# Performance work log

Measured on AMD Instinct MI355X. Metric: run time of the kernel, lower is better.

The kernel has to match this reference:

```python
import jax, jax.numpy as jnp
import numpy as np

B, E, C = 512, 512, 100000
S, M, LAMDA, ALPHA = 30.0, 0.35, 0.01, 0.5  # s, m, lamda from init; ALPHA = args.alpha (center lr)
EPS = 1e-6


def setup_inputs() -> dict:
    key = jax.random.key(0)
    k1, k2, k3, k4 = jax.random.split(key, 4)
    embedding = jax.random.normal(k1, (B, E), dtype=jnp.float32)
    weights = jax.random.normal(k2, (C, E), dtype=jnp.float32)  # kaiming-init classifier weights
    centers = jax.random.normal(k3, (C, E), dtype=jnp.float32)  # class centers buffer
    label = jax.random.randint(k4, (B,), 0, C, dtype=jnp.int64)
    return {"embedding": embedding, "weights": weights, "centers": centers, "label": label}


def reference(embedding, weights, centers, label):
    rows = jnp.arange(B)
    # LMCL (CosFace) logits: cosine similarity via L2-normalized features and weights
    emb_n = embedding / jnp.linalg.norm(embedding, axis=1, keepdims=True)
    w_n = weights / jnp.linalg.norm(weights, axis=1, keepdims=True)
    logits = jnp.einsum('be,ce->bc', emb_n, w_n)            # [B, C]
    # subtract margin m at the target class, then scale by s
    m_logits = S * logits.at[rows, label].add(-M)
    logp = jax.nn.log_softmax(m_logits, axis=1)
    lmcl_loss = -jnp.mean(logp[rows, label])
    # top-1 precision (%)
    prec = jnp.mean((jnp.argmax(m_logits, axis=1) == label).astype(jnp.float32)) * 100.0
    # center loss: MSE between features and their class centers (centers treated as constant)
    centers_batch = centers[label]                           # [B, E] gather
    center_loss = jnp.mean((embedding - centers_batch) ** 2)
    # center update: scatter-subtract mean-normalized diff (replaces the python loop)
    counts = jnp.zeros((C,), dtype=jnp.float32).at[label].add(1.0)
    appear = counts[label]                                   # [B]
    diff = ALPHA * (centers_batch - embedding) / (appear[:, None] + EPS)
    new_centers = centers.at[label].add(-diff)
    total_loss = lmcl_loss + LAMDA * center_loss
    return prec, total_loss, new_centers
```

## Files before the change

### kernel.cpp

```cpp
#include <hip/hip_runtime.h>
#include <cstdint>
#include <cstddef>

#define B_ROWS 512
#define E_DIM  512
#define C_CLS  100000
#define NT     782

#define S_SC    30.0f
#define M_MRG   0.35f
#define LAMBDA_ 0.01f
#define ALPHA_  0.5f
#define EPS_    1e-6f

#define BM 128
#define BN 128
#define BK 64
#define LPAD 8

#define GBN    128
#define GBK    32
#define GSTEPS 16
#define A_GRAN 2048
#define SLOT_GRAN 2560

typedef __attribute__((ext_vector_type(8))) short bf16x8;
typedef __attribute__((ext_vector_type(4))) float f32x4;

static_assert((size_t)NT * GBN >= C_CLS, "tile count");

constexpr size_t WS_PSUM  = 0;
constexpr size_t WS_PMAX  = WS_PSUM + (size_t)NT * B_ROWS * 4;
constexpr size_t WS_CLOSS = WS_PMAX + (size_t)NT * B_ROWS * 4;
constexpr size_t WS_EMBN  = WS_CLOSS + 512;
constexpr size_t WS_IEN   = WS_EMBN + (size_t)B_ROWS * E_DIM * 2;
constexpr size_t WS_COSL  = WS_IEN + 2048;
constexpr size_t WS_CNT   = WS_COSL + 2048;
constexpr size_t WS_RSUM  = WS_CNT + 2048;
constexpr size_t WS_RMAX  = WS_RSUM + 2048;
constexpr size_t WS_WBF   = 4 * 1024 * 1024;
constexpr size_t WS_NEED  = WS_WBF + (size_t)C_CLS * E_DIM * 2;

__device__ __forceinline__ unsigned short f2bf(float f) {
    unsigned u = __float_as_uint(f);
    u += 0x7fffu + ((u >> 16) & 1u);
    return (unsigned short)(u >> 16);
}
__device__ __forceinline__ unsigned fkey(float f) {
    unsigned u = __float_as_uint(f);
    return (u & 0x80000000u) ? ~u : (u | 0x80000000u);
}
__device__ __forceinline__ float unkey(unsigned k) {
    unsigned u = (k & 0x80000000u) ? (k ^ 0x80000000u) : ~k;
    return __uint_as_float(u);
}
__device__ __forceinline__ float waveReduceSum(float v) {
#pragma unroll
    for (int d = 1; d < 64; d <<= 1) v += __shfl_xor(v, d, 64);
    return v;
}
__device__ __forceinline__ unsigned waveReduceMax(unsigned v) {
#pragma unroll
    for (int d = 1; d < 64; d <<= 1) { unsigned o = __shfl_xor(v, d, 64); v = o > v ? o : v; }
    return v;
}
__device__ __forceinline__ float blockReduceSum256(float v, float* s4) {
    v = waveReduceSum(v);
    int w = threadIdx.x >> 6;
    if ((threadIdx.x & 63) == 0) s4[w] = v;
    __syncthreads();
    float r = s4[0] + s4[1] + s4[2] + s4[3];
    __syncthreads();
    return r;
}
__device__ __forceinline__ void g2l16(const void* g, void* l) {
    __builtin_amdgcn_global_load_lds(
        (const __attribute__((address_space(1))) unsigned int*)g,
        (__attribute__((address_space(3))) unsigned int*)l, 16, 0, 0);
}


__global__ __launch_bounds__(256) void emb_prep(const float* __restrict__ emb,
                                                unsigned short* __restrict__ embn,
                                                float* __restrict__ ien) {
    __shared__ float s4[4];
    int b = blockIdx.x, t = threadIdx.x;
    float2 v = *(const float2*)(emb + (size_t)b * E_DIM + t * 2);
    float ss = blockReduceSum256(v.x * v.x + v.y * v.y, s4);
    float inv = 1.0f / sqrtf(ss);
    ushort2 o; o.x = f2bf(v.x * inv); o.y = f2bf(v.y * inv);
    *(ushort2*)(embn + (size_t)b * E_DIM + t * 2) = o;
    if (t == 0) ien[b] = inv;
}

__global__ __launch_bounds__(256) void w_prep(const float* __restrict__ W,
                                              unsigned short* __restrict__ wbf) {
    int row = blockIdx.x * 4 + (threadIdx.x >> 6);
    int lane = threadIdx.x & 63;
    const float* src = W + (size_t)row * E_DIM;
    f32x4 a = *(const f32x4*)(src + lane * 4);
    f32x4 b = *(const f32x4*)(src + 256 + lane * 4);
    float ss = a.x*a.x + a.y*a.y + a.z*a.z + a.w*a.w
             + b.x*b.x + b.y*b.y + b.z*b.z + b.w*b.w;
    ss = waveReduceSum(ss);
    float inv = 1.0f / sqrtf(fmaxf(ss, 1e-30f));
    ushort4 o0, o1;
    o0.x = f2bf(a.x*inv); o0.y = f2bf(a.y*inv); o0.z = f2bf(a.z*inv); o0.w = f2bf(a.w*inv);
    o1.x = f2bf(b.x*inv); o1.y = f2bf(b.y*inv); o1.z = f2bf(b.z*inv); o1.w = f2bf(b.w*inv);
    *(ushort4*)(wbf + (size_t)row * E_DIM + lane * 4) = o0;
    *(ushort4*)(wbf + (size_t)row * E_DIM + 256 + lane * 4) = o1;
}

__global__ __launch_bounds__(256) void label_stats(const float* __restrict__ emb,
                                                   const float* __restrict__ W,
                                                   const float* __restrict__ centers,
                                                   const int* __restrict__ label,
                                                   const float* __restrict__ ien,
                                                   float* __restrict__ cosl,
                                                   float* __restrict__ cntf,
                                                   float* __restrict__ closs) {
    __shared__ float s4[4];
    int b = blockIdx.x, t = threadIdx.x;
    int lab = label[b];
    float d = 0.f, wss = 0.f, sq = 0.f;
    for (int c = t; c < E_DIM; c += 256) {
        float e  = emb[(size_t)b * E_DIM + c];
        float w  = W[(size_t)lab * E_DIM + c];
        float ce = centers[(size_t)lab * E_DIM + c];
        d += e * w; wss += w * w;
        float df = e - ce; sq += df * df;
    }
    float cn = ((label[t] == lab) ? 1.f : 0.f) + ((label[t + 256] == lab) ? 1.f : 0.f);
    d   = blockReduceSum256(d, s4);
    wss = blockReduceSum256(wss, s4);
    sq  = blockReduceSum256(sq, s4);
    cn  = blockReduceSum256(cn, s4);
    if (t == 0) {
        cosl[b] = d * ien[b] / sqrtf(wss);
        cntf[b] = cn;
        atomicAdd(closs, sq);
    }
}

__global__ __launch_bounds__(512, 1) void gemm_fast(const unsigned short* __restrict__ embn,
                                                    const unsigned short* __restrict__ wbf,
                                                    const int* __restrict__ label,
                                                    float* __restrict__ psum,
                                                    unsigned* __restrict__ pmax) {
    __shared__ __align__(16) unsigned short sbuf[3][SLOT_GRAN * 8];
    __shared__ int sLab[B_ROWS];

    const int tid  = threadIdx.x;
    const int lane = tid & 63, wave = tid >> 6;
    const int wm = wave >> 1, wn = wave & 1;
    const int q = lane >> 4, lm = lane & 15;
    const int n0 = blockIdx.x * GBN;

    if (tid < B_ROWS) sLab[tid] = label[tid];

    const int swz = (tid & 3) ^ ((tid >> 3) & 3);
    int aOff[4];
#pragma unroll
    for (int j = 0; j < 4; ++j) {
        int r = j * 128 + (tid >> 2);
        aOff[j] = r * (E_DIM * 2) + swz * 16;
    }
    int rb = n0 + (tid >> 2); if (rb >= C_CLS) rb = 0;
    const size_t bOff = (size_t)rb * (E_DIM * 2) + (size_t)swz * 16;

    const char* aBase = (const char*)embn;
    const char* bBase = (const char*)wbf;

    f32x4 acc[8][4];
#pragma unroll
    for (int i = 0; i < 8; ++i)
#pragma unroll
        for (int j = 0; j < 4; ++j) acc[i][j] = (f32x4){0.f, 0.f, 0.f, 0.f};

#pragma unroll
    for (int s = 0; s < 2; ++s) {
        unsigned short* d = &sbuf[s][0];
        const int kb = s * (GBK * 2);
#pragma unroll
        for (int j = 0; j < 4; ++j)
            g2l16(aBase + aOff[j] + kb, d + (j * 512 + wave * 64) * 8);
        g2l16(bBase + bOff + kb, d + (A_GRAN + wave * 64) * 8);
    }

    const int pq16 = (q ^ ((lm >> 1) & 3)) * 16;

    int sc = 0, ss = 2;
    for (int t = 0; t < GSTEPS; ++t) {
        if (t < GSTEPS - 1)
            asm volatile("s_waitcnt vmcnt(5) lgkmcnt(0)\n\ts_barrier" ::: "memory");
        else
            asm volatile("s_waitcnt vmcnt(0) lgkmcnt(0)\n\ts_barrier" ::: "memory");

        const char* sb = (const char*)&sbuf[sc][0];
        bf16x8 af[8], bfr[4];
#pragma unroll
        for (int i = 0; i < 8; ++i)
            af[i] = *(const bf16x8*)(sb + (wm * 128 + i * 16 + lm) * 64 + pq16);
#pragma unroll
        for (int j = 0; j < 4; ++j)
            bfr[j] = *(const bf16x8*)(sb + A_GRAN * 16 + (wn * 64 + j * 16 + lm) * 64 + pq16);
#pragma unroll
        for (int i = 0; i < 8; ++i)
#pragma unroll
            for (int j = 0; j < 4; ++j)
                acc[i][j] = __builtin_amdgcn_mfma_f32_16x16x32_bf16(af[i], bfr[j], acc[i][j], 0, 0, 0);

        if (t + 2 < GSTEPS) {
            unsigned short* d = &sbuf[ss][0];
            const int kb = (t + 2) * (GBK * 2);
#pragma unroll
            for (int j = 0; j < 4; ++j)
                g2l16(aBase + aOff[j] + kb, d + (j * 512 + wave * 64) * 8);
            g2l16(bBase + bOff + kb, d + (A_GRAN + wave * 64) * 8);
        }
        sc = (sc == 2) ? 0 : sc + 1;
        ss = (ss == 2) ? 0 : ss + 1;
    }

    const size_t pbase = (size_t)blockIdx.x * B_ROWS;
#pragma unroll
    for (int i = 0; i < 8; ++i) {
#pragma unroll
        for (int r = 0; r < 4; ++r) {
            int row = wm * 128 + i * 16 + q * 4 + r;
            int lab = sLab[row];
            float sum = 0.f, mx = -1e30f;
#pragma unroll
            for (int j = 0; j < 4; ++j) {
                int col = n0 + wn * 64 + j * 16 + lm;
                float v = S_SC * acc[i][j][r];
                if (col < C_CLS && col != lab) {
                    sum += __expf(v - 30.0f);
                    mx = fmaxf(mx, v);
                }
            }
#pragma unroll
            for (int d = 1; d < 16; d <<= 1) {
                sum += __shfl_xor(sum, d, 64);
                mx = fmaxf(mx, __shfl_xor(mx, d, 64));
            }
            if (lm == 0) {
                atomicAdd(&psum[pbase + row], sum);
                atomicMax(&pmax[pbase + row], fkey(mx));
            }
        }
    }
}

__global__ __launch_bounds__(256) void gemm_slow(const unsigned short* __restrict__ embn,
                                                 const float* __restrict__ W,
                                                 const int* __restrict__ label,
                                                 float* __restrict__ psum,
                                                 unsigned* __restrict__ pmax) {
    __shared__ __align__(16) unsigned short sA[BM][BK + LPAD];
    __shared__ __align__(16) unsigned short sB[BN][BK + LPAD];
    __shared__ int      sLab[BM];
    __shared__ float    sSum[BM];
    __shared__ unsigned sMax[BM];
    __shared__ float    sInvN[BN];

    const int tid = threadIdx.x;
    const int m0 = blockIdx.x * BM;
    const int n0 = blockIdx.y * BN;
    if (tid < BM) { sLab[tid] = label[m0 + tid]; sSum[tid] = 0.f; sMax[tid] = 0u; }

    const int lane = tid & 63;
    const int wave = tid >> 6;
    const int wm = wave >> 1, wn = wave & 1;
    const int q = lane >> 4, lm = lane & 15;

    const int arow = tid >> 3, ac8 = tid & 7;
    const int brow = tid >> 4, bc4 = tid & 15;

    f32x4 acc[4][4];
#pragma unroll
    for (int i = 0; i < 4; ++i)
#pragma unroll
        for (int j = 0; j < 4; ++j) acc[i][j] = (f32x4){0.f, 0.f, 0.f, 0.f};

    float rss[8];
#pragma unroll
    for (int j = 0; j < 8; ++j) rss[j] = 0.f;

    const float* wb = W + (size_t)(n0 + brow) * E_DIM + bc4 * 4;

    for (int k0 = 0; k0 < E_DIM; k0 += BK) {
        __syncthreads();
#pragma unroll
        for (int j = 0; j < 4; ++j) {
            int rr = arow + 32 * j;
            uint4 v = *(const uint4*)(embn + (size_t)(m0 + rr) * E_DIM + k0 + ac8 * 8);
            *(uint4*)(&sA[rr][ac8 * 8]) = v;
        }
#pragma unroll
        for (int j = 0; j < 8; ++j) {
            int rr = brow + 16 * j;
            f32x4 v = (f32x4){0.f, 0.f, 0.f, 0.f};
            if (n0 + rr < C_CLS) v = *(const f32x4*)(wb + (size_t)(16 * j) * E_DIM + k0);
            rss[j] += v.x * v.x + v.y * v.y + v.z * v.z + v.w * v.w;
            ushort4 o; o.x = f2bf(v.x); o.y = f2bf(v.y); o.z = f2bf(v.z); o.w = f2bf(v.w);
            *(ushort4*)(&sB[rr][bc4 * 4]) = o;
        }
        __syncthreads();
#pragma unroll
        for (int kk = 0; kk < BK; kk += 32) {
            bf16x8 af[4], bfr[4];
#pragma unroll
            for (int i = 0; i < 4; ++i)
                af[i] = *(const bf16x8*)(&sA[wm * 64 + i * 16 + lm][kk + q * 8]);
#pragma unroll
            for (int j = 0; j < 4; ++j)
                bfr[j] = *(const bf16x8*)(&sB[wn * 64 + j * 16 + lm][kk + q * 8]);
#pragma unroll
            for (int i = 0; i < 4; ++i)
#pragma unroll
                for (int j = 0; j < 4; ++j)
                    acc[i][j] = __builtin_amdgcn_mfma_f32_16x16x32_bf16(af[i], bfr[j], acc[i][j], 0, 0, 0);
        }
    }
#pragma unroll
    for (int j = 0; j < 8; ++j) {
        float v = rss[j];
#pragma unroll
        for (int d = 1; d < 16; d <<= 1) v += __shfl_xor(v, d, 64);
        if (bc4 == 0) sInvN[brow + 16 * j] = rsqrtf(fmaxf(v, 1e-30f));
    }
    __syncthreads();
#pragma unroll
    for (int i = 0; i < 4; ++i) {
#pragma unroll
        for (int r = 0; r < 4; ++r) {
            int row_l = wm * 64 + i * 16 + q * 4 + r;
            int lab = sLab[row_l];
            float sum = 0.f, mx = -1e30f;
#pragma unroll
            for (int j = 0; j < 4; ++j) {
                int col_l = wn * 64 + j * 16 + lm;
                int col = n0 + col_l;
                float v = S_SC * acc[i][j][r] * sInvN[col_l];
                if (col < C_CLS && col != lab) {
                    sum += __expf(v - 30.0f);
                    mx = fmaxf(mx, v);
                }
            }
#pragma unroll
            for (int d = 1; d < 16; d <<= 1) {
                sum += __shfl_xor(sum, d, 64);
                mx = fmaxf(mx, __shfl_xor(mx, d, 64));
            }
            if (lm == 0) {
                atomicAdd(&sSum[row_l], sum);
                atomicMax(&sMax[row_l], fkey(mx));
            }
        }
    }
    __syncthreads();
    if (tid < BM) {
        psum[(size_t)blockIdx.y * B_ROWS + m0 + tid] = sSum[tid];
        pmax[(size_t)blockIdx.y * B_ROWS + m0 + tid] = sMax[tid];
    }
}

__global__ __launch_bounds__(256) void row_reduce(const float* __restrict__ psum,
                                                  const unsigned* __restrict__ pmax,
                                                  float* __restrict__ rsum,
                                                  float* __restrict__ rmax) {
    __shared__ float s4[4];
    __shared__ unsigned m4[4];
    int b = blockIdx.x, t = threadIdx.x;
    float s = 0.f; unsigned mk = 0u;
    for (int nt = t; nt < NT; nt += 256) {
        s += psum[(size_t)nt * B_ROWS + b];
        unsigned k = pmax[(size_t)nt * B_ROWS + b];
        mk = k > mk ? k : mk;
    }
    s = waveReduceSum(s);
    mk = waveReduceMax(mk);
    int w = t >> 6;
    if ((t & 63) == 0) { s4[w] = s; m4[w] = mk; }
    __syncthreads();
    if (t == 0) {
        rsum[b] = s4[0] + s4[1] + s4[2] + s4[3];
        unsigned m = m4[0];
#pragma unroll
        for (int i = 1; i < 4; ++i) m = m4[i] > m ? m4[i] : m;
        rmax[b] = unkey(m);
    }
}

__global__ __launch_bounds__(256) void finalize(const float* __restrict__ cosl,
                                                const float* __restrict__ rsum,
                                                const float* __restrict__ rmax,
                                                const float* __restrict__ closs,
                                                float* __restrict__ out) {
    __shared__ float s4[4];
    int t = threadIdx.x;
    float lsum = 0.f, msum = 0.f;
    for (int b = t; b < B_ROWS; b += 256) {
        float lv = S_SC * (cosl[b] - M_MRG);
        float tot = rsum[b] + __expf(lv - 30.0f);
        lsum += (logf(tot) + 30.0f) - lv;
        msum += (lv > rmax[b]) ? 1.0f : 0.0f;
    }
    lsum = blockReduceSum256(lsum, s4);
    msum = blockReduceSum256(msum, s4);
    if (t == 0) {
        out[0] = msum * (100.0f / (float)B_ROWS);
        out[1] = lsum * (1.0f / (float)B_ROWS)
               + LAMBDA_ * closs[0] * (1.0f / ((float)B_ROWS * (float)E_DIM));
    }
}

__global__ __launch_bounds__(256) void centers_copy(const float* __restrict__ src,
                                                    float* __restrict__ dst) {
    size_t i = (size_t)blockIdx.x * blockDim.x + threadIdx.x;
    size_t stride = (size_t)gridDim.x * blockDim.x;
    constexpr size_t N  = (size_t)C_CLS * E_DIM;
    constexpr size_t n4 = (N - 2) / 4;
    const float2* s2 = (const float2*)(src + 2);
    float4* d4 = (float4*)(dst + 2);
    for (size_t k = i; k < n4; k += stride) {
        float2 a = s2[2 * k], b = s2[2 * k + 1];
        d4[k] = make_float4(a.x, a.y, b.x, b.y);
    }
    if (i == 0) {
        *(float2*)dst = *(const float2*)src;
        constexpr size_t t0 = 2 + 4 * n4;
        *(float2*)(dst + t0) = *(const float2*)(src + t0);
    }
}

__global__ __launch_bounds__(256) void scatter_upd(const float* __restrict__ emb,
                                                   const float* __restrict__ centers,
                                                   const int* __restrict__ label,
                                                   const float* __restrict__ cntf,
                                                   float* __restrict__ outC) {
    int b = blockIdx.x, t = threadIdx.x;
    int lab = label[b];
    float sc = ALPHA_ / (cntf[b] + EPS_);
    for (int c = t; c < E_DIM; c += 256) {
        float add = sc * (emb[(size_t)b * E_DIM + c] - centers[(size_t)lab * E_DIM + c]);
        atomicAdd(outC + (size_t)lab * E_DIM + c, add);
    }
}

extern "C" void kernel_launch(void* const* d_in, const int* in_sizes, int n_in,
                              void* d_out, int out_size, void* d_ws, size_t ws_size,
                              hipStream_t stream) {
    const float* emb     = (const float*)d_in[0];
    const float* W       = (const float*)d_in[1];
    const float* centers = (const float*)d_in[2];
    const int*   label   = (const int*)d_in[3];
    float* out = (float*)d_out;
    char* ws = (char*)d_ws;

    float*          psum = (float*)(ws + WS_PSUM);
    unsigned*       pmax = (unsigned*)(ws + WS_PMAX);
    float*          closs = (float*)(ws + WS_CLOSS);
    unsigned short* embn = (unsigned short*)(ws + WS_EMBN);
    float*          ien  = (float*)(ws + WS_IEN);
    float*          cosl = (float*)(ws + WS_COSL);
    float*          cntf = (float*)(ws + WS_CNT);
    float*          rsum = (float*)(ws + WS_RSUM);
    float*          rmax = (float*)(ws + WS_RMAX);
    unsigned short* wbf  = (unsigned short*)(ws + WS_WBF);

    hipMemsetAsync(ws, 0, WS_CLOSS + 512, stream);

    emb_prep<<<B_ROWS, 256, 0, stream>>>(emb, embn, ien);
    label_stats<<<B_ROWS, 256, 0, stream>>>(emb, W, centers, label, ien, cosl, cntf, closs);
    if (ws_size >= WS_NEED) {
        w_prep<<<C_CLS / 4, 256, 0, stream>>>(W, wbf);
        gemm_fast<<<NT, 512, 0, stream>>>(embn, wbf, label, psum, pmax);
    } else {
        gemm_slow<<<dim3(B_ROWS / BM, NT), 256, 0, stream>>>(embn, W, label, psum, pmax);
    }
    row_reduce<<<B_ROWS, 256, 0, stream>>>(psum, pmax, rsum, rmax);
    finalize<<<1, 256, 0, stream>>>(cosl, rsum, rmax, closs, out);
    centers_copy<<<12500, 256, 0, stream>>>(centers, out + 2);
    scatter_upd<<<B_ROWS, 256, 0, stream>>>(emb, centers, label, cntf, out + 2);
}
```

Baseline: 602.5 us.

## Fuse weight normalization and centers copy into GEMM, drop bf16 weight prepass

```diff
diff --git a/kernel.cpp b/kernel.cpp
--- a/kernel.cpp
+++ b/kernel.cpp
@@ -13,16 +13,8 @@
 #define ALPHA_  0.5f
 #define EPS_    1e-6f
 
-#define BM 128
-#define BN 128
-#define BK 64
-#define LPAD 8
-
 #define GBN    128
-#define GBK    32
 #define GSTEPS 16
-#define A_GRAN 2048
-#define SLOT_GRAN 2560
 
 typedef __attribute__((ext_vector_type(8))) short bf16x8;
 typedef __attribute__((ext_vector_type(4))) float f32x4;
@@ -33,13 +25,10 @@
 constexpr size_t WS_PMAX  = WS_PSUM + (size_t)NT * B_ROWS * 4;
 constexpr size_t WS_CLOSS = WS_PMAX + (size_t)NT * B_ROWS * 4;
 constexpr size_t WS_EMBN  = WS_CLOSS + 512;
-constexpr size_t WS_IEN   = WS_EMBN + (size_t)B_ROWS * E_DIM * 2;
-constexpr size_t WS_COSL  = WS_IEN + 2048;
+constexpr size_t WS_COSL  = WS_EMBN + (size_t)B_ROWS * E_DIM * 2;
 constexpr size_t WS_CNT   = WS_COSL + 2048;
 constexpr size_t WS_RSUM  = WS_CNT + 2048;
 constexpr size_t WS_RMAX  = WS_RSUM + 2048;
-constexpr size_t WS_WBF   = 4 * 1024 * 1024;
-constexpr size_t WS_NEED  = WS_WBF + (size_t)C_CLS * E_DIM * 2;
 
 __device__ __forceinline__ unsigned short f2bf(float f) {
     unsigned u = __float_as_uint(f);
@@ -73,82 +62,55 @@
     __syncthreads();
     return r;
 }
-__device__ __forceinline__ void g2l16(const void* g, void* l) {
-    __builtin_amdgcn_global_load_lds(
-        (const __attribute__((address_space(1))) unsigned int*)g,
-        (__attribute__((address_space(3))) unsigned int*)l, 16, 0, 0);
-}
-
-
-__global__ __launch_bounds__(256) void emb_prep(const float* __restrict__ emb,
-                                                unsigned short* __restrict__ embn,
-                                                float* __restrict__ ien) {
-    __shared__ float s4[4];
-    int b = blockIdx.x, t = threadIdx.x;
-    float2 v = *(const float2*)(emb + (size_t)b * E_DIM + t * 2);
-    float ss = blockReduceSum256(v.x * v.x + v.y * v.y, s4);
-    float inv = 1.0f / sqrtf(ss);
-    ushort2 o; o.x = f2bf(v.x * inv); o.y = f2bf(v.y * inv);
-    *(ushort2*)(embn + (size_t)b * E_DIM + t * 2) = o;
-    if (t == 0) ien[b] = inv;
-}
-
-__global__ __launch_bounds__(256) void w_prep(const float* __restrict__ W,
-                                              unsigned short* __restrict__ wbf) {
-    int row = blockIdx.x * 4 + (threadIdx.x >> 6);
-    int lane = threadIdx.x & 63;
-    const float* src = W + (size_t)row * E_DIM;
-    f32x4 a = *(const f32x4*)(src + lane * 4);
-    f32x4 b = *(const f32x4*)(src + 256 + lane * 4);
-    float ss = a.x*a.x + a.y*a.y + a.z*a.z + a.w*a.w
-             + b.x*b.x + b.y*b.y + b.z*b.z + b.w*b.w;
-    ss = waveReduceSum(ss);
-    float inv = 1.0f / sqrtf(fmaxf(ss, 1e-30f));
-    ushort4 o0, o1;
-    o0.x = f2bf(a.x*inv); o0.y = f2bf(a.y*inv); o0.z = f2bf(a.z*inv); o0.w = f2bf(a.w*inv);
-    o1.x = f2bf(b.x*inv); o1.y = f2bf(b.y*inv); o1.z = f2bf(b.z*inv); o1.w = f2bf(b.w*inv);
-    *(ushort4*)(wbf + (size_t)row * E_DIM + lane * 4) = o0;
-    *(ushort4*)(wbf + (size_t)row * E_DIM + 256 + lane * 4) = o1;
-}
-
-__global__ __launch_bounds__(256) void label_stats(const float* __restrict__ emb,
-                                                   const float* __restrict__ W,
-                                                   const float* __restrict__ centers,
-                                                   const int* __restrict__ label,
-                                                   const float* __restrict__ ien,
-                                                   float* __restrict__ cosl,
-                                                   float* __restrict__ cntf,
-                                                   float* __restrict__ closs) {
+
+
+__global__ __launch_bounds__(256) void prep_stats(const float* __restrict__ emb,
+                                                  const float* __restrict__ W,
+                                                  const float* __restrict__ centers,
+                                                  const int* __restrict__ label,
+                                                  unsigned short* __restrict__ embn,
+                                                  float* __restrict__ cosl,
+                                                  float* __restrict__ cntf,
+                                                  float* __restrict__ closs) {
     __shared__ float s4[4];
     int b = blockIdx.x, t = threadIdx.x;
     int lab = label[b];
-    float d = 0.f, wss = 0.f, sq = 0.f;
-    for (int c = t; c < E_DIM; c += 256) {
-        float e  = emb[(size_t)b * E_DIM + c];
-        float w  = W[(size_t)lab * E_DIM + c];
-        float ce = centers[(size_t)lab * E_DIM + c];
-        d += e * w; wss += w * w;
-        float df = e - ce; sq += df * df;
-    }
+    float2 e2 = *(const float2*)(emb     + (size_t)b   * E_DIM + t * 2);
+    float2 w2 = *(const float2*)(W       + (size_t)lab * E_DIM + t * 2);
+    float2 c2 = *(const float2*)(centers + (size_t)lab * E_DIM + t * 2);
+    float ssq = e2.x * e2.x + e2.y * e2.y;
+    float d   = e2.x * w2.x + e2.y * w2.y;
+    float wss = w2.x * w2.x + w2.y * w2.y;
+    float dx = e2.x - c2.x, dy = e2.y - c2.y;
+    float sq  = dx * dx + dy * dy;
     float cn = ((label[t] == lab) ? 1.f : 0.f) + ((label[t + 256] == lab) ? 1.f : 0.f);
-    d   = blockReduceSum256(d, s4);
+    ssq = blockReduceSum256(ssq, s4);
+    d   = blockReduceSum256(d,   s4);
     wss = blockReduceSum256(wss, s4);
-    sq  = blockReduceSum256(sq, s4);
-    cn  = blockReduceSum256(cn, s4);
+    sq  = blockReduceSum256(sq,  s4);
+    cn  = blockReduceSum256(cn,  s4);
+    float inv = 1.0f / sqrtf(ssq);
+    ushort2 o; o.x = f2bf(e2.x * inv); o.y = f2bf(e2.y * inv);
+    *(ushort2*)(embn + (size_t)b * E_DIM + t * 2) = o;
     if (t == 0) {
-        cosl[b] = d * ien[b] / sqrtf(wss);
+        cosl[b] = d * inv / sqrtf(wss);
         cntf[b] = cn;
         atomicAdd(closs, sq);
     }
 }
 
-__global__ __launch_bounds__(512, 1) void gemm_fast(const unsigned short* __restrict__ embn,
-                                                    const unsigned short* __restrict__ wbf,
-                                                    const int* __restrict__ label,
-                                                    float* __restrict__ psum,
-                                                    unsigned* __restrict__ pmax) {
-    __shared__ __align__(16) unsigned short sbuf[3][SLOT_GRAN * 8];
-    __shared__ int sLab[B_ROWS];
+__global__ __launch_bounds__(512, 1) void gemm_fused(const unsigned short* __restrict__ embn,
+                                                     const float* __restrict__ W,
+                                                     const int* __restrict__ label,
+                                                     float* __restrict__ psum,
+                                                     unsigned* __restrict__ pmax,
+                                                     const float* __restrict__ centers,
+                                                     float* __restrict__ outC,
+                                                     unsigned* __restrict__ ctr) {
+    __shared__ __align__(16) unsigned short sB[2][GBN * 32];
+    __shared__ int      sLab[B_ROWS];
+    __shared__ float    sInv[GBN];
+    __shared__ unsigned sChunk;
 
     const int tid  = threadIdx.x;
     const int lane = tid & 63, wave = tid >> 6;
@@ -156,20 +118,26 @@
     const int q = lane >> 4, lm = lane & 15;
     const int n0 = blockIdx.x * GBN;
 
-    if (tid < B_ROWS) sLab[tid] = label[tid];
-
-    const int swz = (tid & 3) ^ ((tid >> 3) & 3);
-    int aOff[4];
+    sLab[tid & (B_ROWS - 1)] = label[tid & (B_ROWS - 1)];
+
+    const int brow = tid >> 2;
+    const int bl   = tid & 3;
+    int brg = n0 + brow; if (brg >= C_CLS) brg = 0;
+    const float* bsrc = W + (size_t)brg * E_DIM + bl * 8;
+    const int bphys = bl ^ ((brow >> 1) & 3);
+    unsigned short* bwr = &sB[0][brow * 32 + bphys * 8];
+
+    const unsigned short* aP[8];
+#pragma unroll
+    for (int i = 0; i < 8; ++i)
+        aP[i] = embn + (size_t)(wm * 128 + i * 16 + lm) * E_DIM + q * 8;
+
+    const unsigned short* brd[4];
 #pragma unroll
     for (int j = 0; j < 4; ++j) {
-        int r = j * 128 + (tid >> 2);
-        aOff[j] = r * (E_DIM * 2) + swz * 16;
-    }
-    int rb = n0 + (tid >> 2); if (rb >= C_CLS) rb = 0;
-    const size_t bOff = (size_t)rb * (E_DIM * 2) + (size_t)swz * 16;
-
-    const char* aBase = (const char*)embn;
-    const char* bBase = (const char*)wbf;
+        int row = wn * 64 + j * 16 + lm;
+        brd[j] = &sB[0][row * 32 + (q ^ ((row >> 1) & 3)) * 8];
+    }
 
     f32x4 acc[8][4];
 #pragma unroll
@@ -177,50 +145,78 @@
 #pragma unroll
         for (int j = 0; j < 4; ++j) acc[i][j] = (f32x4){0.f, 0.f, 0.f, 0.f};
 
-#pragma unroll
-    for (int s = 0; s < 2; ++s) {
-        unsigned short* d = &sbuf[s][0];
-        const int kb = s * (GBK * 2);
-#pragma unroll
-        for (int j = 0; j < 4; ++j)
-            g2l16(aBase + aOff[j] + kb, d + (j * 512 + wave * 64) * 8);
-        g2l16(bBase + bOff + kb, d + (A_GRAN + wave * 64) * 8);
-    }
-
-    const int pq16 = (q ^ ((lm >> 1) & 3)) * 16;
-
-    int sc = 0, ss = 2;
-    for (int t = 0; t < GSTEPS; ++t) {
-        if (t < GSTEPS - 1)
-            asm volatile("s_waitcnt vmcnt(5) lgkmcnt(0)\n\ts_barrier" ::: "memory");
-        else
-            asm volatile("s_waitcnt vmcnt(0) lgkmcnt(0)\n\ts_barrier" ::: "memory");
-
-        const char* sb = (const char*)&sbuf[sc][0];
-        bf16x8 af[8], bfr[4];
-#pragma unroll
-        for (int i = 0; i < 8; ++i)
-            af[i] = *(const bf16x8*)(sb + (wm * 128 + i * 16 + lm) * 64 + pq16);
-#pragma unroll
-        for (int j = 0; j < 4; ++j)
-            bfr[j] = *(const bf16x8*)(sb + A_GRAN * 16 + (wn * 64 + j * 16 + lm) * 64 + pq16);
-#pragma unroll
-        for (int i = 0; i < 8; ++i)
-#pragma unroll
-            for (int j = 0; j < 4; ++j)
-                acc[i][j] = __builtin_amdgcn_mfma_f32_16x16x32_bf16(af[i], bfr[j], acc[i][j], 0, 0, 0);
-
-        if (t + 2 < GSTEPS) {
-            unsigned short* d = &sbuf[ss][0];
-            const int kb = (t + 2) * (GBK * 2);
-#pragma unroll
-            for (int j = 0; j < 4; ++j)
-                g2l16(aBase + aOff[j] + kb, d + (j * 512 + wave * 64) * 8);
-            g2l16(bBase + bOff + kb, d + (A_GRAN + wave * 64) * 8);
-        }
-        sc = (sc == 2) ? 0 : sc + 1;
-        ss = (ss == 2) ? 0 : ss + 1;
-    }
+    float ss = 0.f;
+    f32x4 bA0, bA1, bB0, bB1;
+
+    bA0 = *(const f32x4*)(bsrc + 0);
+    bA1 = *(const f32x4*)(bsrc + 4);
+    bB0 = *(const f32x4*)(bsrc + 32);
+    bB1 = *(const f32x4*)(bsrc + 36);
+    {
+        ss += bA0.x*bA0.x + bA0.y*bA0.y + bA0.z*bA0.z + bA0.w*bA0.w
+            + bA1.x*bA1.x + bA1.y*bA1.y + bA1.z*bA1.z + bA1.w*bA1.w;
+        bf16x8 o;
+        o[0] = (short)f2bf(bA0.x); o[1] = (short)f2bf(bA0.y);
+        o[2] = (short)f2bf(bA0.z); o[3] = (short)f2bf(bA0.w);
+        o[4] = (short)f2bf(bA1.x); o[5] = (short)f2bf(bA1.y);
+        o[6] = (short)f2bf(bA1.z); o[7] = (short)f2bf(bA1.w);
+        *(bf16x8*)bwr = o;
+    }
+    asm volatile("s_waitcnt lgkmcnt(0)" ::: "memory");
+    __builtin_amdgcn_sched_barrier(0);
+    __builtin_amdgcn_s_barrier();
+
+#define STEP(T, WR0, WR1, LD0, LD1)                                             \
+    {                                                                           \
+        const int t_ = (T);                                                     \
+        bf16x8 af[8];                                                           \
+        _Pragma("unroll")                                                       \
+        for (int i = 0; i < 8; ++i)                                             \
+            af[i] = *(const bf16x8*)(aP[i] + t_ * 32);                          \
+        if (t_ + 2 < GSTEPS) {                                                  \
+            LD0 = *(const f32x4*)(bsrc + (t_ + 2) * 32);                        \
+            LD1 = *(const f32x4*)(bsrc + (t_ + 2) * 32 + 4);                    \
+        }                                                                       \
+        if (t_ + 1 < GSTEPS) {                                                  \
+            ss += WR0.x*WR0.x + WR0.y*WR0.y + WR0.z*WR0.z + WR0.w*WR0.w         \
+                + WR1.x*WR1.x + WR1.y*WR1.y + WR1.z*WR1.z + WR1.w*WR1.w;        \
+            bf16x8 o;                                                           \
+            o[0] = (short)f2bf(WR0.x); o[1] = (short)f2bf(WR0.y);               \
+            o[2] = (short)f2bf(WR0.z); o[3] = (short)f2bf(WR0.w);               \
+            o[4] = (short)f2bf(WR1.x); o[5] = (short)f2bf(WR1.y);               \
+            o[6] = (short)f2bf(WR1.z); o[7] = (short)f2bf(WR1.w);               \
+            *(bf16x8*)(bwr + ((t_ + 1) & 1) * 4096) = o;                        \
+        }                                                                       \
+        bf16x8 bfr[4];                                                          \
+        _Pragma("unroll")                                                       \
+        for (int j = 0; j < 4; ++j)                                             \
+            bfr[j] = *(const bf16x8*)(brd[j] + (t_ & 1) * 4096);                \
+        _Pragma("unroll")                                                       \
+        for (int i = 0; i < 8; ++i)                                             \
+            _Pragma("unroll")                                                   \
+            for (int j = 0; j < 4; ++j)                                         \
+                acc[i][j] = __builtin_amdgcn_mfma_f32_16x16x32_bf16(af[i], bfr[j], acc[i][j], 0, 0, 0); \
+        __builtin_amdgcn_sched_barrier(0);                                      \
+        asm volatile("s_waitcnt lgkmcnt(0)" ::: "memory");                      \
+        __builtin_amdgcn_sched_barrier(0);                                      \
+        __builtin_amdgcn_s_barrier();                                           \
+    }
+
+#pragma unroll
+    for (int tt = 0; tt < GSTEPS; tt += 2) {
+        STEP(tt,     bB0, bB1, bA0, bA1);
+        STEP(tt + 1, bA0, bA1, bB0, bB1);
+    }
+#undef STEP
+
+    ss += __shfl_xor(ss, 1, 64);
+    ss += __shfl_xor(ss, 2, 64);
+    if ((tid & 3) == 0) sInv[brow] = rsqrtf(fmaxf(ss, 1e-30f));
+    __syncthreads();
+
+    float inv_j[4];
+#pragma unroll
+    for (int j = 0; j < 4; ++j) inv_j[j] = sInv[wn * 64 + j * 16 + lm];
 
     const size_t pbase = (size_t)blockIdx.x * B_ROWS;
 #pragma unroll
@@ -233,7 +229,7 @@
 #pragma unroll
             for (int j = 0; j < 4; ++j) {
                 int col = n0 + wn * 64 + j * 16 + lm;
-                float v = S_SC * acc[i][j][r];
+                float v = S_SC * acc[i][j][r] * inv_j[j];
                 if (col < C_CLS && col != lab) {
                     sum += __expf(v - 30.0f);
                     mx = fmaxf(mx, v);
@@ -250,119 +246,31 @@
             }
         }
     }
-}
-
-__global__ __launch_bounds__(256) void gemm_slow(const unsigned short* __restrict__ embn,
-                                                 const float* __restrict__ W,
-                                                 const int* __restrict__ label,
-                                                 float* __restrict__ psum,
-                                                 unsigned* __restrict__ pmax) {
-    __shared__ __align__(16) unsigned short sA[BM][BK + LPAD];
-    __shared__ __align__(16) unsigned short sB[BN][BK + LPAD];
-    __shared__ int      sLab[BM];
-    __shared__ float    sSum[BM];
-    __shared__ unsigned sMax[BM];
-    __shared__ float    sInvN[BN];
-
-    const int tid = threadIdx.x;
-    const int m0 = blockIdx.x * BM;
-    const int n0 = blockIdx.y * BN;
-    if (tid < BM) { sLab[tid] = label[m0 + tid]; sSum[tid] = 0.f; sMax[tid] = 0u; }
-
-    const int lane = tid & 63;
-    const int wave = tid >> 6;
-    const int wm = wave >> 1, wn = wave & 1;
-    const int q = lane >> 4, lm = lane & 15;
-
-    const int arow = tid >> 3, ac8 = tid & 7;
-    const int brow = tid >> 4, bc4 = tid & 15;
-
-    f32x4 acc[4][4];
-#pragma unroll
-    for (int i = 0; i < 4; ++i)
-#pragma unroll
-        for (int j = 0; j < 4; ++j) acc[i][j] = (f32x4){0.f, 0.f, 0.f, 0.f};
-
-    float rss[8];
-#pragma unroll
-    for (int j = 0; j < 8; ++j) rss[j] = 0.f;
-
-    const float* wb = W + (size_t)(n0 + brow) * E_DIM + bc4 * 4;
-
-    for (int k0 = 0; k0 < E_DIM; k0 += BK) {
+
+    constexpr size_t N4 = ((size_t)C_CLS * E_DIM - 2) / 4;
+    constexpr unsigned NCHUNK = (unsigned)((N4 + 4095) / 4096);
+    const float2* s2 = (const float2*)(centers + 2);
+    float4* d4 = (float4*)(outC + 2);
+    for (;;) {
+        if (tid == 0) sChunk = atomicAdd(ctr, 1u);
         __syncthreads();
-#pragma unroll
-        for (int j = 0; j < 4; ++j) {
-            int rr = arow + 32 * j;
-            uint4 v = *(const uint4*)(embn + (size_t)(m0 + rr) * E_DIM + k0 + ac8 * 8);
-            *(uint4*)(&sA[rr][ac8 * 8]) = v;
-        }
-#pragma unroll
-        for (int j = 0; j < 8; ++j) {
-            int rr = brow + 16 * j;
-            f32x4 v = (f32x4){0.f, 0.f, 0.f, 0.f};
-            if (n0 + rr < C_CLS) v = *(const f32x4*)(wb + (size_t)(16 * j) * E_DIM + k0);
-            rss[j] += v.x * v.x + v.y * v.y + v.z * v.z + v.w * v.w;
-            ushort4 o; o.x = f2bf(v.x); o.y = f2bf(v.y); o.z = f2bf(v.z); o.w = f2bf(v.w);
-            *(ushort4*)(&sB[rr][bc4 * 4]) = o;
-        }
+        unsigned c = sChunk;
         __syncthreads();
-#pragma unroll
-        for (int kk = 0; kk < BK; kk += 32) {
-            bf16x8 af[4], bfr[4];
-#pragma unroll
-            for (int i = 0; i < 4; ++i)
-                af[i] = *(const bf16x8*)(&sA[wm * 64 + i * 16 + lm][kk + q * 8]);
-#pragma unroll
-            for (int j = 0; j < 4; ++j)
-                bfr[j] = *(const bf16x8*)(&sB[wn * 64 + j * 16 + lm][kk + q * 8]);
-#pragma unroll
-            for (int i = 0; i < 4; ++i)
-#pragma unroll
-                for (int j = 0; j < 4; ++j)
-                    acc[i][j] = __builtin_amdgcn_mfma_f32_16x16x32_bf16(af[i], bfr[j], acc[i][j], 0, 0, 0);
-        }
-    }
-#pragma unroll
-    for (int j = 0; j < 8; ++j) {
-        float v = rss[j];
-#pragma unroll
-        for (int d = 1; d < 16; d <<= 1) v += __shfl_xor(v, d, 64);
-        if (bc4 == 0) sInvN[brow + 16 * j] = rsqrtf(fmaxf(v, 1e-30f));
-    }
-    __syncthreads();
-#pragma unroll
-    for (int i = 0; i < 4; ++i) {
-#pragma unroll
-        for (int r = 0; r < 4; ++r) {
-            int row_l = wm * 64 + i * 16 + q * 4 + r;
-            int lab = sLab[row_l];
-            float sum = 0.f, mx = -1e30f;
-#pragma unroll
-            for (int j = 0; j < 4; ++j) {
-                int col_l = wn * 64 + j * 16 + lm;
-                int col = n0 + col_l;
-                float v = S_SC * acc[i][j][r] * sInvN[col_l];
-                if (col < C_CLS && col != lab) {
-                    sum += __expf(v - 30.0f);
-                    mx = fmaxf(mx, v);
-                }
-            }
-#pragma unroll
-            for (int d = 1; d < 16; d <<= 1) {
-                sum += __shfl_xor(sum, d, 64);
-                mx = fmaxf(mx, __shfl_xor(mx, d, 64));
-            }
-            if (lm == 0) {
-                atomicAdd(&sSum[row_l], sum);
-                atomicMax(&sMax[row_l], fkey(mx));
+        if (c >= NCHUNK) break;
+        size_t g0 = (size_t)c * 4096;
+#pragma unroll
+        for (int u = 0; u < 8; ++u) {
+            size_t g = g0 + (size_t)u * 512 + tid;
+            if (g < N4) {
+                float2 a = s2[2 * g], b = s2[2 * g + 1];
+                d4[g] = make_float4(a.x, a.y, b.x, b.y);
             }
         }
-    }
-    __syncthreads();
-    if (tid < BM) {
-        psum[(size_t)blockIdx.y * B_ROWS + m0 + tid] = sSum[tid];
-        pmax[(size_t)blockIdx.y * B_ROWS + m0 + tid] = sMax[tid];
+        if (c == 0 && tid == 0) {
+            *(float2*)outC = *(const float2*)centers;
+            constexpr size_t t0 = 2 + 4 * N4;
+            *(float2*)(outC + t0) = *(const float2*)(centers + t0);
+        }
     }
 }
 
@@ -416,25 +324,6 @@
     }
 }
 
-__global__ __launch_bounds__(256) void centers_copy(const float* __restrict__ src,
-                                                    float* __restrict__ dst) {
-    size_t i = (size_t)blockIdx.x * blockDim.x + threadIdx.x;
-    size_t stride = (size_t)gridDim.x * blockDim.x;
-    constexpr size_t N  = (size_t)C_CLS * E_DIM;
-    constexpr size_t n4 = (N - 2) / 4;
-    const float2* s2 = (const float2*)(src + 2);
-    float4* d4 = (float4*)(dst + 2);
-    for (size_t k = i; k < n4; k += stride) {
-        float2 a = s2[2 * k], b = s2[2 * k + 1];
-        d4[k] = make_float4(a.x, a.y, b.x, b.y);
-    }
-    if (i == 0) {
-        *(float2*)dst = *(const float2*)src;
-        constexpr size_t t0 = 2 + 4 * n4;
-        *(float2*)(dst + t0) = *(const float2*)(src + t0);
-    }
-}
-
 __global__ __launch_bounds__(256) void scatter_upd(const float* __restrict__ emb,
                                                    const float* __restrict__ centers,
                                                    const int* __restrict__ label,
@@ -462,26 +351,18 @@
     float*          psum = (float*)(ws + WS_PSUM);
     unsigned*       pmax = (unsigned*)(ws + WS_PMAX);
     float*          closs = (float*)(ws + WS_CLOSS);
+    unsigned*       ctr  = (unsigned*)(ws + WS_CLOSS + 8);
     unsigned short* embn = (unsigned short*)(ws + WS_EMBN);
-    float*          ien  = (float*)(ws + WS_IEN);
     float*          cosl = (float*)(ws + WS_COSL);
     float*          cntf = (float*)(ws + WS_CNT);
     float*          rsum = (float*)(ws + WS_RSUM);
     float*          rmax = (float*)(ws + WS_RMAX);
-    unsigned short* wbf  = (unsigned short*)(ws + WS_WBF);
-
-    hipMemsetAsync(ws, 0, WS_CLOSS + 512, stream);
-
-    emb_prep<<<B_ROWS, 256, 0, stream>>>(emb, embn, ien);
-    label_stats<<<B_ROWS, 256, 0, stream>>>(emb, W, centers, label, ien, cosl, cntf, closs);
-    if (ws_size >= WS_NEED) {
-        w_prep<<<C_CLS / 4, 256, 0, stream>>>(W, wbf);
-        gemm_fast<<<NT, 512, 0, stream>>>(embn, wbf, label, psum, pmax);
-    } else {
-        gemm_slow<<<dim3(B_ROWS / BM, NT), 256, 0, stream>>>(embn, W, label, psum, pmax);
-    }
+
+    (void)hipMemsetAsync(ws, 0, WS_CLOSS + 512, stream);
+
+    prep_stats<<<B_ROWS, 256, 0, stream>>>(emb, W, centers, label, embn, cosl, cntf, closs);
+    gemm_fused<<<NT, 512, 0, stream>>>(embn, W, label, psum, pmax, centers, out + 2, ctr);
     row_reduce<<<B_ROWS, 256, 0, stream>>>(psum, pmax, rsum, rmax);
     finalize<<<1, 256, 0, stream>>>(cosl, rsum, rmax, closs, out);
-    centers_copy<<<12500, 256, 0, stream>>>(centers, out + 2);
     scatter_upd<<<B_ROWS, 256, 0, stream>>>(emb, centers, label, cntf, out + 2);
 }
```

Measured after the change: 617.4 us. 1.02x slower.
